# Kernel optimization log

Measured on AMD Instinct MI355X. Metric: run time of the kernel, lower is better.

## Reference

```python
import jax, jax.numpy as jnp
import numpy as np

TOP_K = 2


def setup_inputs() -> dict:
    key = jax.random.key(0)
    ks = jax.random.split(key, 5)
    B, S, H, E, F = 4, 1024, 1024, 16, 4096
    scale = 0.02
    return {
        "input_tensor": jax.random.normal(ks[0], (B, S, H), dtype=jnp.float32),
        "Wg": scale * jax.random.normal(ks[1], (H, E), dtype=jnp.float32),
        "bg": jnp.zeros((E,), dtype=jnp.float32),
        "W1": scale * jax.random.normal(ks[2], (E, H, F), dtype=jnp.float32),
        "b1": jnp.zeros((E, F), dtype=jnp.float32),
        "W2": scale * jax.random.normal(ks[3], (E, F, H), dtype=jnp.float32),
        "b2": jnp.zeros((E, H), dtype=jnp.float32),
    }


def reference(input_tensor, Wg, bg, W1, b1, W2, b2):
    # Faithful to DualOutputMoE.forward_first_pass: the per-(b,s,k) Python loop
    # plus _weighted_sum collapses ALL token expert outputs into a single
    # [1,1,H] vector normalized by the total routing weight (= B*S).
    B, S, H = input_tensor.shape
    T = B * S
    E = Wg.shape[1]
    x = input_tensor.reshape(T, H)

    routing_scores = x @ Wg + bg                    # [T, E] (raw gate logits)
    top_v, top_i = jax.lax.top_k(routing_scores, TOP_K)
    top_w = jax.nn.softmax(top_v, axis=-1)          # per-token top-k weights

    # combine[t, e] = sum_k top_w[t, k] * 1[top_i[t, k] == e]
    combine = jnp.zeros((T, E), x.dtype).at[jnp.arange(T)[:, None], top_i].add(top_w)
    total_weight = top_w.sum()                      # matches python sum of .item()s

    def expert_step(acc, params):
        w1, bb1, w2, bb2, c = params                # c: [T] combine weights for this expert
        y = jax.nn.gelu(x @ w1 + bb1, approximate=False) @ w2 + bb2  # [T, H]
        return acc + c @ y, None

    acc0 = jnp.zeros((H,), x.dtype)
    acc, _ = jax.lax.scan(expert_step, acc0, (W1, b1, W2, b2, combine.T))
    first_output = (acc / total_weight).reshape(1, 1, H)
    return first_output
```

## Files before the change

kernel.cpp:

```cpp
#include <hip/hip_runtime.h>
#include <hip/hip_bf16.h>
#include <math.h>

typedef __bf16 bf16_t;
typedef __bf16 bf16x4 __attribute__((ext_vector_type(4)));
typedef __bf16 bf16x8 __attribute__((ext_vector_type(8)));
typedef float  f32x4  __attribute__((ext_vector_type(4)));

#define T_TOK 4096
#define H_DIM 1024
#define E_NUM 16
#define F_DIM 4096
#define CH_MAX 16

#define WS_E0     0
#define WS_E1     16384
#define WS_W0     32768
#define WS_W1     49152
#define WS_COUNTS 65536
#define WS_SUMW   65792
#define WS_LIDX   131072
#define WS_LW     393216
#define WS_GPART  655360
#define WS_G      4849664
#define WS_P2     5105664

__global__ __launch_bounds__(64) void k_route(const float* __restrict__ x,
    const float* __restrict__ Wg, const float* __restrict__ bg,
    int* __restrict__ e0, int* __restrict__ e1,
    float* __restrict__ w0, float* __restrict__ w1)
{
    const int t = blockIdx.x;
    const int lane = threadIdx.x;
    const float* xr = x + (size_t)t * H_DIM;

    float s[E_NUM];
#pragma unroll
    for (int e = 0; e < E_NUM; ++e) s[e] = 0.f;

#pragma unroll
    for (int i = 0; i < 16; ++i) {
        const int h = i * 64 + lane;
        const float xv = xr[h];
        const float4* wr = (const float4*)(Wg + (size_t)h * E_NUM);
        float4 q0 = wr[0], q1 = wr[1], q2 = wr[2], q3 = wr[3];
        s[0] += xv*q0.x;  s[1] += xv*q0.y;  s[2] += xv*q0.z;  s[3] += xv*q0.w;
        s[4] += xv*q1.x;  s[5] += xv*q1.y;  s[6] += xv*q1.z;  s[7] += xv*q1.w;
        s[8] += xv*q2.x;  s[9] += xv*q2.y;  s[10]+= xv*q2.z;  s[11]+= xv*q2.w;
        s[12]+= xv*q3.x;  s[13]+= xv*q3.y;  s[14]+= xv*q3.z;  s[15]+= xv*q3.w;
    }
#pragma unroll
    for (int off = 32; off >= 1; off >>= 1) {
#pragma unroll
        for (int e = 0; e < E_NUM; ++e) s[e] += __shfl_xor(s[e], off);
    }
    if (lane == 0) {
#pragma unroll
        for (int e = 0; e < E_NUM; ++e) s[e] += bg[e];
        float b1v = -3e38f; int i1 = 0;
#pragma unroll
        for (int e = 0; e < E_NUM; ++e) { if (s[e] > b1v) { b1v = s[e]; i1 = e; } }
        float b2v = -3e38f; int i2 = 0;
#pragma unroll
        for (int e = 0; e < E_NUM; ++e) { if (e != i1 && s[e] > b2v) { b2v = s[e]; i2 = e; } }
        const float ex  = expf(b2v - b1v);
        const float inv = 1.f / (1.f + ex);
        e0[t] = i1; e1[t] = i2;
        w0[t] = inv; w1[t] = ex * inv;
    }
}

__global__ __launch_bounds__(64) void k_lists(const int* __restrict__ e0, const int* __restrict__ e1,
    const float* __restrict__ w0, const float* __restrict__ w1,
    int* __restrict__ lidx, float* __restrict__ lw,
    int* __restrict__ counts, float* __restrict__ sumw)
{
    const int e = blockIdx.x;
    const int lane = threadIdx.x;
    int cnt = 0; float sw = 0.f;
    for (int base = 0; base < T_TOK; base += 64) {
        const int t = base + lane;
        const bool m0 = (e0[t] == e);
        const bool m1 = (e1[t] == e);
        const bool m  = m0 | m1;
        const unsigned long long bal = __ballot(m);
        const int pos = cnt + __popcll(bal & ((1ull << lane) - 1ull));
        if (m) {
            const float w = m0 ? w0[t] : w1[t];
            lidx[e * T_TOK + pos] = t;
            lw[e * T_TOK + pos]   = w;
            sw += w;
        }
        cnt += __popcll(bal);
    }
#pragma unroll
    for (int off = 32; off >= 1; off >>= 1) sw += __shfl_xor(sw, off);
    if (lane == 0) { counts[e] = cnt; sumw[e] = sw; }
}

__global__ __launch_bounds__(512) void k_expert(const float* __restrict__ x,
    const float* __restrict__ W1, const float* __restrict__ b1,
    const int* __restrict__ lidx, const float* __restrict__ lw,
    const int* __restrict__ counts, float* __restrict__ gpart)
{
    const int ftile = blockIdx.x;
    const int chunk = blockIdx.y;
    const int e     = blockIdx.z;
    const int cnt   = counts[e];
    const int start = chunk * 256;
    if (chunk > 0 && start >= cnt) return;
    int valid = cnt - start;
    if (valid > 256) valid = 256;
    if (valid < 0)   valid = 0;

    __shared__ bf16_t Alds[256][40];
    __shared__ bf16_t Blds[64][40];
    __shared__ int    tok_s[256];
    __shared__ float  w_s[256];
    __shared__ float  b1_s[64];
    __shared__ float  gred[4][64];

    const int tid = threadIdx.x;
    if (tid < 256) {
        const int r = start + tid;
        const bool ok = (tid < valid);
        tok_s[tid] = ok ? lidx[e * T_TOK + r] : 0;
        w_s[tid]   = ok ? lw[e * T_TOK + r]   : 0.f;
    } else if (tid < 320) {
        const int f = tid - 256;
        b1_s[f] = b1[(size_t)e * F_DIM + ftile * 64 + f];
    }
    __syncthreads();

    const int lane = tid & 63;
    const int wid  = tid >> 6;
    const int wm   = wid & 3;
    const int wn   = wid >> 2;
    const int lr   = lane & 15;
    const int lg   = lane >> 4;

    f32x4 acc[4][2];
#pragma unroll
    for (int i = 0; i < 4; ++i)
#pragma unroll
        for (int j = 0; j < 2; ++j)
#pragma unroll
            for (int q = 0; q < 4; ++q) acc[i][j][q] = 0.f;

    const float* W1e = W1 + (size_t)e * H_DIM * F_DIM + (size_t)ftile * 64;

    const int arow0 = tid >> 3;
    const int aquad = tid & 7;
    const int bf    = tid & 63;
    const int bk0   = tid >> 6;

    for (int k0 = 0; k0 < H_DIM; k0 += 32) {
#pragma unroll
        for (int p = 0; p < 4; ++p) {
            const int row = arow0 + p * 64;
            const float4 v = *(const float4*)(x + (size_t)tok_s[row] * H_DIM + k0 + aquad * 4);
            bf16x4 bv;
            bv[0] = (bf16_t)v.x; bv[1] = (bf16_t)v.y; bv[2] = (bf16_t)v.z; bv[3] = (bf16_t)v.w;
            *(bf16x4*)&Alds[row][aquad * 4] = bv;
        }
#pragma unroll
        for (int p = 0; p < 4; ++p) {
            const int k = bk0 + p * 8;
            const float v = W1e[(size_t)(k0 + k) * F_DIM + bf];
            Blds[bf][k] = (bf16_t)v;
        }
        __syncthreads();

        bf16x8 afrag[4], bfrag[2];
#pragma unroll
        for (int mf = 0; mf < 4; ++mf)
            afrag[mf] = *(const bf16x8*)&Alds[wm * 64 + mf * 16 + lr][lg * 8];
#pragma unroll
        for (int nf = 0; nf < 2; ++nf)
            bfrag[nf] = *(const bf16x8*)&Blds[wn * 32 + nf * 16 + lr][lg * 8];
#pragma unroll
        for (int mf = 0; mf < 4; ++mf)
#pragma unroll
            for (int nf = 0; nf < 2; ++nf)
                acc[mf][nf] = __builtin_amdgcn_mfma_f32_16x16x32_bf16(afrag[mf], bfrag[nf], acc[mf][nf], 0, 0, 0);
        __syncthreads();
    }

    float gcol[2] = {0.f, 0.f};
#pragma unroll
    for (int nf = 0; nf < 2; ++nf) {
        const float bb = b1_s[wn * 32 + nf * 16 + lr];
#pragma unroll
        for (int mf = 0; mf < 4; ++mf) {
#pragma unroll
            for (int i = 0; i < 4; ++i) {
                const int row = wm * 64 + mf * 16 + lg * 4 + i;
                const float h  = acc[mf][nf][i] + bb;
                const float gl = 0.5f * h * (1.f + erff(h * 0.70710678118654752f));
                gcol[nf] += w_s[row] * gl;
            }
        }
    }
#pragma unroll
    for (int nf = 0; nf < 2; ++nf) {
        gcol[nf] += __shfl_xor(gcol[nf], 16);
        gcol[nf] += __shfl_xor(gcol[nf], 32);
    }
    if (lane < 16) {
#pragma unroll
        for (int nf = 0; nf < 2; ++nf)
            gred[wm][wn * 32 + nf * 16 + lane] = gcol[nf];
    }
    __syncthreads();
    if (tid < 64) {
        const float sum = gred[0][tid] + gred[1][tid] + gred[2][tid] + gred[3][tid];
        gpart[(size_t)(e * CH_MAX + chunk) * F_DIM + ftile * 64 + tid] = sum;
    }
}

__global__ __launch_bounds__(256) void k_redg(const float* __restrict__ gpart,
    const int* __restrict__ counts, float* __restrict__ g)
{
    const int e = blockIdx.y;
    const int f = blockIdx.x * 256 + threadIdx.x;
    const int nch = (counts[e] + 255) >> 8;
    float s = 0.f;
    for (int c = 0; c < nch; ++c)
        s += gpart[(size_t)(e * CH_MAX + c) * F_DIM + f];
    g[(size_t)e * F_DIM + f] = s;
}

__global__ __launch_bounds__(256) void k_out1(const float* __restrict__ g,
    const float* __restrict__ W2, float* __restrict__ p2)
{
    const int fc = blockIdx.x;
    const int e  = blockIdx.y;
    const int tid = threadIdx.x;
    __shared__ float gs[128];
    if (tid < 128) gs[tid] = g[(size_t)e * F_DIM + fc * 128 + tid];
    __syncthreads();
    const float* W2p = W2 + (size_t)e * F_DIM * H_DIM + (size_t)fc * 128 * H_DIM;
    float ax = 0.f, ay = 0.f, az = 0.f, aw = 0.f;
#pragma unroll 4
    for (int f = 0; f < 128; ++f) {
        const float gv = gs[f];
        const float4 wv = *(const float4*)(W2p + (size_t)f * H_DIM + tid * 4);
        ax += gv * wv.x; ay += gv * wv.y; az += gv * wv.z; aw += gv * wv.w;
    }
    float4 st; st.x = ax; st.y = ay; st.z = az; st.w = aw;
    *(float4*)(p2 + (size_t)(e * 32 + fc) * H_DIM + tid * 4) = st;
}

__global__ __launch_bounds__(256) void k_out2(const float* __restrict__ p2,
    const float* __restrict__ sumw, const float* __restrict__ b2, float* __restrict__ out)
{
    const int tid = threadIdx.x;
    const int hh  = tid & 31;
    const int seg = tid >> 5;
    const int h   = blockIdx.x * 32 + hh;
    float s = 0.f;
    for (int j = 0; j < 64; ++j)
        s += p2[(size_t)(seg * 64 + j) * H_DIM + h];
    __shared__ float red[8][33];
    red[seg][hh] = s;
    __syncthreads();
    if (tid < 32) {
        const int h2 = blockIdx.x * 32 + tid;
        float tot = 0.f;
#pragma unroll
        for (int q = 0; q < 8; ++q) tot += red[q][tid];
        float tw = 0.f, bias = 0.f;
#pragma unroll
        for (int e = 0; e < E_NUM; ++e) { tw += sumw[e]; bias += sumw[e] * b2[e * H_DIM + h2]; }
        out[h2] = (tot + bias) / tw;
    }
}

extern "C" void kernel_launch(void* const* d_in, const int* in_sizes, int n_in,
                              void* d_out, int out_size, void* d_ws, size_t ws_size,
                              hipStream_t stream) {
    const float* x  = (const float*)d_in[0];
    const float* Wg = (const float*)d_in[1];
    const float* bg = (const float*)d_in[2];
    const float* W1 = (const float*)d_in[3];
    const float* b1 = (const float*)d_in[4];
    const float* W2 = (const float*)d_in[5];
    const float* b2 = (const float*)d_in[6];
    float* out = (float*)d_out;

    char* ws = (char*)d_ws;
    int*   e0     = (int*)(ws + WS_E0);
    int*   e1     = (int*)(ws + WS_E1);
    float* w0     = (float*)(ws + WS_W0);
    float* w1     = (float*)(ws + WS_W1);
    int*   counts = (int*)(ws + WS_COUNTS);
    float* sumw   = (float*)(ws + WS_SUMW);
    int*   lidx   = (int*)(ws + WS_LIDX);
    float* lw     = (float*)(ws + WS_LW);
    float* gpart  = (float*)(ws + WS_GPART);
    float* g      = (float*)(ws + WS_G);
    float* p2     = (float*)(ws + WS_P2);

    k_route<<<T_TOK, 64, 0, stream>>>(x, Wg, bg, e0, e1, w0, w1);
    k_lists<<<E_NUM, 64, 0, stream>>>(e0, e1, w0, w1, lidx, lw, counts, sumw);
    k_expert<<<dim3(F_DIM / 64, CH_MAX, E_NUM), 512, 0, stream>>>(x, W1, b1, lidx, lw, counts, gpart);
    k_redg<<<dim3(F_DIM / 256, E_NUM), 256, 0, stream>>>(gpart, counts, g);
    k_out1<<<dim3(32, E_NUM), 256, 0, stream>>>(g, W2, p2);
    k_out2<<<32, 256, 0, stream>>>(p2, sumw, b2, out);
}
```

Measured before the change: 375.1 us.

## Pre-gather routed tokens to swizzled bf16 buffer and use direct-to-LDS loads

Adds a scan kernel computing padded per-expert offsets and a gather kernel that writes each expert's routed token rows once as bf16 in an XOR-swizzled layout. The expert GEMM then streams A tiles with global_load_lds straight into LDS, uses a 64-deep K step, 256 threads with 4x4 MFMA tiles per wave, and reads W1 as 16 strided values per thread packed into bf16. This removes the repeated fp32 gather and conversion of x across all 64 F tiles and cuts bank conflicts. In exchange it adds two launches and an extra bf16 copy of the routed activations in workspace.

After: 383.8 us. 1.02x slower.

```diff
diff --git a/kernel.cpp b/kernel.cpp
--- a/kernel.cpp
+++ b/kernel.cpp
@@ -18,12 +18,17 @@
 #define WS_W0     32768
 #define WS_W1     49152
 #define WS_COUNTS 65536
-#define WS_SUMW   65792
+#define WS_SUMW   65664
+#define WS_XOFF   65792
 #define WS_LIDX   131072
 #define WS_LW     393216
 #define WS_GPART  655360
 #define WS_G      4849664
-#define WS_P2     5105664
+#define WS_P2     5111808
+#define WS_XE     7208960
+
+#define AS_GLOBAL(p) ((const __attribute__((address_space(1))) void*)(p))
+#define AS_LDS(p)    ((__attribute__((address_space(3))) void*)(p))
 
 __global__ __launch_bounds__(64) void k_route(const float* __restrict__ x,
     const float* __restrict__ Wg, const float* __restrict__ bg,
@@ -98,103 +103,139 @@
     if (lane == 0) { counts[e] = cnt; sumw[e] = sw; }
 }
 
-__global__ __launch_bounds__(512) void k_expert(const float* __restrict__ x,
+__global__ void k_scan(const int* __restrict__ counts, int* __restrict__ xoff) {
+    if (threadIdx.x == 0) {
+        int o = 0;
+        for (int e = 0; e < E_NUM; ++e) { xoff[e] = o; o += (counts[e] + 255) & ~255; }
+    }
+}
+
+__global__ __launch_bounds__(256) void k_gather(const float* __restrict__ x,
+    const int* __restrict__ lidx, const int* __restrict__ counts,
+    const int* __restrict__ xoff, bf16_t* __restrict__ Xe)
+{
+    const int chunk = blockIdx.x, e = blockIdx.y;
+    const int cnt = counts[e];
+    const int start = chunk * 256;
+    if (chunk && start >= cnt) return;
+    const int tid = threadIdx.x;
+    const size_t rbase = (size_t)xoff[e] + start;
+
+    for (int it = 0; it < 128; ++it) {
+        const int task = it * 256 + tid;
+        const int rl   = task >> 7;
+        const int sc   = task & 127;
+        const int row  = start + rl;
+        bf16x8 v8 = {};
+        if (row < cnt) {
+            const int tok = lidx[e * T_TOK + row];
+            const int l   = (sc & 7) ^ (rl & 7);
+            const int k   = (sc >> 3) * 64 + l * 8;
+            const float4 a = *(const float4*)(x + (size_t)tok * H_DIM + k);
+            const float4 b = *(const float4*)(x + (size_t)tok * H_DIM + k + 4);
+            v8[0]=(bf16_t)a.x; v8[1]=(bf16_t)a.y; v8[2]=(bf16_t)a.z; v8[3]=(bf16_t)a.w;
+            v8[4]=(bf16_t)b.x; v8[5]=(bf16_t)b.y; v8[6]=(bf16_t)b.z; v8[7]=(bf16_t)b.w;
+        }
+        *(bf16x8*)(Xe + (rbase + rl) * H_DIM + sc * 8) = v8;
+    }
+}
+
+__global__ __launch_bounds__(256, 2) void k_expert(
     const float* __restrict__ W1, const float* __restrict__ b1,
-    const int* __restrict__ lidx, const float* __restrict__ lw,
-    const int* __restrict__ counts, float* __restrict__ gpart)
+    const bf16_t* __restrict__ Xe, const float* __restrict__ lw,
+    const int* __restrict__ counts, const int* __restrict__ xoff,
+    float* __restrict__ gpart)
 {
     const int ftile = blockIdx.x;
     const int chunk = blockIdx.y;
     const int e     = blockIdx.z;
     const int cnt   = counts[e];
     const int start = chunk * 256;
-    if (chunk > 0 && start >= cnt) return;
-    int valid = cnt - start;
-    if (valid > 256) valid = 256;
-    if (valid < 0)   valid = 0;
-
-    __shared__ bf16_t Alds[256][40];
-    __shared__ bf16_t Blds[64][40];
-    __shared__ int    tok_s[256];
-    __shared__ float  w_s[256];
-    __shared__ float  b1_s[64];
-    __shared__ float  gred[4][64];
-
-    const int tid = threadIdx.x;
-    if (tid < 256) {
-        const int r = start + tid;
-        const bool ok = (tid < valid);
-        tok_s[tid] = ok ? lidx[e * T_TOK + r] : 0;
-        w_s[tid]   = ok ? lw[e * T_TOK + r]   : 0.f;
-    } else if (tid < 320) {
-        const int f = tid - 256;
-        b1_s[f] = b1[(size_t)e * F_DIM + ftile * 64 + f];
-    }
-    __syncthreads();
-
+    if (chunk && start >= cnt) return;
+
+    __shared__ __align__(16) bf16_t Alds[256 * 64];
+    __shared__ __align__(16) bf16_t Blds[64 * 72];
+    __shared__ float w_s[256];
+    __shared__ float b1_s[64];
+    __shared__ float gred[4][64];
+
+    const int tid  = threadIdx.x;
     const int lane = tid & 63;
     const int wid  = tid >> 6;
-    const int wm   = wid & 3;
-    const int wn   = wid >> 2;
     const int lr   = lane & 15;
     const int lg   = lane >> 4;
 
-    f32x4 acc[4][2];
+    {
+        const int r = start + tid;
+        w_s[tid] = (r < cnt) ? lw[e * T_TOK + r] : 0.f;
+        if (tid < 64) b1_s[tid] = b1[(size_t)e * F_DIM + ftile * 64 + tid];
+    }
+
+    f32x4 acc[4][4];
 #pragma unroll
     for (int i = 0; i < 4; ++i)
 #pragma unroll
-        for (int j = 0; j < 2; ++j)
+        for (int j = 0; j < 4; ++j)
 #pragma unroll
             for (int q = 0; q < 4; ++q) acc[i][j][q] = 0.f;
 
-    const float* W1e = W1 + (size_t)e * H_DIM * F_DIM + (size_t)ftile * 64;
-
-    const int arow0 = tid >> 3;
-    const int aquad = tid & 7;
-    const int bf    = tid & 63;
-    const int bk0   = tid >> 6;
-
-    for (int k0 = 0; k0 < H_DIM; k0 += 32) {
-#pragma unroll
-        for (int p = 0; p < 4; ++p) {
-            const int row = arow0 + p * 64;
-            const float4 v = *(const float4*)(x + (size_t)tok_s[row] * H_DIM + k0 + aquad * 4);
-            bf16x4 bv;
-            bv[0] = (bf16_t)v.x; bv[1] = (bf16_t)v.y; bv[2] = (bf16_t)v.z; bv[3] = (bf16_t)v.w;
-            *(bf16x4*)&Alds[row][aquad * 4] = bv;
-        }
-#pragma unroll
-        for (int p = 0; p < 4; ++p) {
-            const int k = bk0 + p * 8;
-            const float v = W1e[(size_t)(k0 + k) * F_DIM + bf];
-            Blds[bf][k] = (bf16_t)v;
+    const bf16_t* Asrc = Xe + ((size_t)xoff[e] + start) * H_DIM;
+    const float* W1p = W1 + (size_t)e * H_DIM * F_DIM + (size_t)ftile * 64 + lane;
+
+    for (int k0 = 0; k0 < H_DIM; k0 += 64) {
+#pragma unroll
+        for (int p = 0; p < 8; ++p) {
+            const int seg = wid * 8 + p;
+            const int r   = seg * 8 + (lane >> 3);
+            const int c   = lane & 7;
+            const bf16_t* src = Asrc + (size_t)r * H_DIM + k0 + c * 8;
+            __builtin_amdgcn_global_load_lds(AS_GLOBAL(src),
+                AS_LDS((char*)Alds + seg * 1024), 16, 0, 0);
+        }
+        {
+            const float* wp = W1p + (size_t)(k0 + wid * 16) * F_DIM;
+            float bv[16];
+#pragma unroll
+            for (int j = 0; j < 16; ++j) bv[j] = wp[(size_t)j * F_DIM];
+            bf16x8 pk0, pk1;
+#pragma unroll
+            for (int q = 0; q < 8; ++q) { pk0[q] = (bf16_t)bv[q]; pk1[q] = (bf16_t)bv[8 + q]; }
+            bf16_t* bdst = &Blds[lane * 72 + wid * 16];
+            *(bf16x8*)bdst       = pk0;
+            *(bf16x8*)(bdst + 8) = pk1;
         }
         __syncthreads();
 
-        bf16x8 afrag[4], bfrag[2];
-#pragma unroll
-        for (int mf = 0; mf < 4; ++mf)
-            afrag[mf] = *(const bf16x8*)&Alds[wm * 64 + mf * 16 + lr][lg * 8];
-#pragma unroll
-        for (int nf = 0; nf < 2; ++nf)
-            bfrag[nf] = *(const bf16x8*)&Blds[wn * 32 + nf * 16 + lr][lg * 8];
-#pragma unroll
-        for (int mf = 0; mf < 4; ++mf)
-#pragma unroll
-            for (int nf = 0; nf < 2; ++nf)
-                acc[mf][nf] = __builtin_amdgcn_mfma_f32_16x16x32_bf16(afrag[mf], bfrag[nf], acc[mf][nf], 0, 0, 0);
+#pragma unroll
+        for (int kh = 0; kh < 2; ++kh) {
+            bf16x8 af[4], bfr[4];
+#pragma unroll
+            for (int mf = 0; mf < 4; ++mf) {
+                const int r = wid * 64 + mf * 16 + lr;
+                const int eoff = (kh * 32 + lg * 8) ^ ((r & 7) * 8);
+                af[mf] = *(const bf16x8*)&Alds[r * 64 + eoff];
+            }
+#pragma unroll
+            for (int nf = 0; nf < 4; ++nf)
+                bfr[nf] = *(const bf16x8*)&Blds[(nf * 16 + lr) * 72 + kh * 32 + lg * 8];
+#pragma unroll
+            for (int mf = 0; mf < 4; ++mf)
+#pragma unroll
+                for (int nf = 0; nf < 4; ++nf)
+                    acc[mf][nf] = __builtin_amdgcn_mfma_f32_16x16x32_bf16(af[mf], bfr[nf], acc[mf][nf], 0, 0, 0);
+        }
         __syncthreads();
     }
 
-    float gcol[2] = {0.f, 0.f};
-#pragma unroll
-    for (int nf = 0; nf < 2; ++nf) {
-        const float bb = b1_s[wn * 32 + nf * 16 + lr];
+    float gcol[4] = {0.f, 0.f, 0.f, 0.f};
+#pragma unroll
+    for (int nf = 0; nf < 4; ++nf) {
+        const float bb = b1_s[nf * 16 + lr];
 #pragma unroll
         for (int mf = 0; mf < 4; ++mf) {
 #pragma unroll
             for (int i = 0; i < 4; ++i) {
-                const int row = wm * 64 + mf * 16 + lg * 4 + i;
+                const int row = wid * 64 + mf * 16 + lg * 4 + i;
                 const float h  = acc[mf][nf][i] + bb;
                 const float gl = 0.5f * h * (1.f + erff(h * 0.70710678118654752f));
                 gcol[nf] += w_s[row] * gl;
@@ -202,14 +243,13 @@
         }
     }
 #pragma unroll
-    for (int nf = 0; nf < 2; ++nf) {
+    for (int nf = 0; nf < 4; ++nf) {
         gcol[nf] += __shfl_xor(gcol[nf], 16);
         gcol[nf] += __shfl_xor(gcol[nf], 32);
     }
     if (lane < 16) {
 #pragma unroll
-        for (int nf = 0; nf < 2; ++nf)
-            gred[wm][wn * 32 + nf * 16 + lane] = gcol[nf];
+        for (int nf = 0; nf < 4; ++nf) gred[wid][nf * 16 + lane] = gcol[nf];
     }
     __syncthreads();
     if (tid < 64) {
@@ -289,21 +329,25 @@
     float* out = (float*)d_out;
 
     char* ws = (char*)d_ws;
-    int*   e0     = (int*)(ws + WS_E0);
-    int*   e1     = (int*)(ws + WS_E1);
-    float* w0     = (float*)(ws + WS_W0);
-    float* w1     = (float*)(ws + WS_W1);
-    int*   counts = (int*)(ws + WS_COUNTS);
-    float* sumw   = (float*)(ws + WS_SUMW);
-    int*   lidx   = (int*)(ws + WS_LIDX);
-    float* lw     = (float*)(ws + WS_LW);
-    float* gpart  = (float*)(ws + WS_GPART);
-    float* g      = (float*)(ws + WS_G);
-    float* p2     = (float*)(ws + WS_P2);
+    int*    e0     = (int*)(ws + WS_E0);
+    int*    e1     = (int*)(ws + WS_E1);
+    float*  w0     = (float*)(ws + WS_W0);
+    float*  w1     = (float*)(ws + WS_W1);
+    int*    counts = (int*)(ws + WS_COUNTS);
+    float*  sumw   = (float*)(ws + WS_SUMW);
+    int*    xoff   = (int*)(ws + WS_XOFF);
+    int*    lidx   = (int*)(ws + WS_LIDX);
+    float*  lw     = (float*)(ws + WS_LW);
+    float*  gpart  = (float*)(ws + WS_GPART);
+    float*  g      = (float*)(ws + WS_G);
+    float*  p2     = (float*)(ws + WS_P2);
+    bf16_t* Xe     = (bf16_t*)(ws + WS_XE);
 
     k_route<<<T_TOK, 64, 0, stream>>>(x, Wg, bg, e0, e1, w0, w1);
     k_lists<<<E_NUM, 64, 0, stream>>>(e0, e1, w0, w1, lidx, lw, counts, sumw);
-    k_expert<<<dim3(F_DIM / 64, CH_MAX, E_NUM), 512, 0, stream>>>(x, W1, b1, lidx, lw, counts, gpart);
+    k_scan<<<1, 64, 0, stream>>>(counts, xoff);
+    k_gather<<<dim3(CH_MAX, E_NUM), 256, 0, stream>>>(x, lidx, counts, xoff, Xe);
+    k_expert<<<dim3(F_DIM / 64, CH_MAX, E_NUM), 256, 0, stream>>>(W1, b1, Xe, lw, counts, xoff, gpart);
     k_redg<<<dim3(F_DIM / 256, E_NUM), 256, 0, stream>>>(gpart, counts, g);
     k_out1<<<dim3(32, E_NUM), 256, 0, stream>>>(g, W2, p2);
     k_out2<<<32, 256, 0, stream>>>(p2, sumw, b2, out);
```
